# Kernel tuning notes

Measured on AMD Instinct MI355X. Metric: run time of the kernel, lower is better.

The kernel has to match this reference:

```python
import jax, jax.numpy as jnp
import numpy as np

B, H, W, C = 16, 64, 64, 256
WIN, SHIFT, HEADS, NSTYLE, HID = 8, 4, 8, 512, 1024
HB = HEADS // 2   # heads per attention branch
CB = C // 2       # channels per branch
N = WIN * WIN     # tokens per window
EPS = 1e-5


def _rel_index(w):
    coords = np.stack(np.meshgrid(np.arange(w), np.arange(w), indexing='ij'))  # [2,w,w]
    cf = coords.reshape(2, -1)
    rel = (cf[:, :, None] - cf[:, None, :]).transpose(1, 2, 0)  # [N,N,2]
    rel[:, :, 0] += w - 1
    rel[:, :, 1] += w - 1
    rel[:, :, 0] *= 2 * w - 1
    return rel.sum(-1)  # [N,N]


def _sw_mask(Hh, Ww, w, shift):
    img = np.zeros((Hh, Ww))
    cnt = 0
    for hs in (slice(0, -w), slice(-w, -shift), slice(-shift, None)):
        for ws in (slice(0, -w), slice(-w, -shift), slice(-shift, None)):
            img[hs, ws] = cnt
            cnt += 1
    win = img.reshape(Hh // w, w, Ww // w, w).transpose(0, 2, 1, 3).reshape(-1, w * w)
    m = win[:, None, :] - win[:, :, None]
    return np.where(m != 0, -100.0, 0.0).astype(np.float32)  # [nW,N,N]


REL_IDX = _rel_index(WIN)
SW_MASK = jnp.asarray(_sw_mask(H, W, WIN, SHIFT))


def window_partition(x):
    # x: [B,H,W,c] -> [B*nW, N, c]
    b, hh, ww, c = x.shape
    x = x.reshape(b, hh // WIN, WIN, ww // WIN, WIN, c).transpose(0, 1, 3, 2, 4, 5)
    return x.reshape(-1, N, c)


def window_reverse(win):
    c = win.shape[-1]
    x = win.reshape(B, H // WIN, W // WIN, WIN, WIN, c).transpose(0, 1, 3, 2, 4, 5)
    return x.reshape(B, H, W, c)


def _adain(x, style, Wa, ba):
    # x: [B,L,C]; instance norm over L per channel, then style affine
    s = style @ Wa + ba                      # [B, 2C]
    mu_s, std_s = jnp.split(s, 2, axis=1)    # each [B,C]
    mu = x.mean(axis=1, keepdims=True)
    var = ((x - mu) ** 2).mean(axis=1, keepdims=True)
    xn = (x - mu) * jax.lax.rsqrt(var + EPS)
    return mu_s[:, None, :] + std_s[:, None, :] * xn


def _win_attn(q, k, v, rpb, mask):
    # q,k,v: [B_, N, CB]; rpb: [(2w-1)^2, HB]; mask: [nW,N,N] or None
    B_ = q.shape[0]
    d = CB // HB
    q = q.reshape(B_, N, HB, d).transpose(0, 2, 1, 3) * (d ** -0.5)
    k = k.reshape(B_, N, HB, d).transpose(0, 2, 1, 3)
    v = v.reshape(B_, N, HB, d).transpose(0, 2, 1, 3)
    attn = jnp.einsum('bhnd,bhmd->bhnm', q, k)
    bias = rpb[REL_IDX.reshape(-1)].reshape(N, N, HB).transpose(2, 0, 1)
    attn = attn + bias[None]
    if mask is not None:
        nW = mask.shape[0]
        attn = attn.reshape(B_ // nW, nW, HB, N, N) + mask[None, :, None]
        attn = attn.reshape(B_, HB, N, N)
    attn = jax.nn.softmax(attn, axis=-1)
    out = jnp.einsum('bhnm,bhmd->bhnd', attn, v)
    return out.transpose(0, 2, 1, 3).reshape(B_, N, CB)


def setup_inputs() -> dict:
    key = jax.random.key(0)
    ks = jax.random.split(key, 20)
    f = jnp.float32
    return {
        'x': jax.random.normal(ks[0], (B, H * W, C), f),
        'style': jax.random.normal(ks[1], (B, NSTYLE), f),
        'w_qkv': jax.random.normal(ks[2], (C, 3 * C), f) * 0.02,
        'b_qkv': jnp.zeros((3 * C,), f),
        'w_proj': jax.random.normal(ks[3], (C, C), f) * 0.02,
        'b_proj': jnp.zeros((C,), f),
        'w_ada1': jax.random.normal(ks[4], (NSTYLE, 2 * C), f) * 0.02,
        'b_ada1': jnp.concatenate([jnp.zeros((C,), f), jnp.ones((C,), f)]),
        'w_ada2': jax.random.normal(ks[5], (NSTYLE, 2 * C), f) * 0.02,
        'b_ada2': jnp.concatenate([jnp.zeros((C,), f), jnp.ones((C,), f)]),
        'rpb1': jax.random.normal(ks[6], ((2 * WIN - 1) ** 2, HB), f) * 0.02,
        'rpb2': jax.random.normal(ks[7], ((2 * WIN - 1) ** 2, HB), f) * 0.02,
        'w_fc1': jax.random.normal(ks[8], (C, HID), f) * 0.02,
        'b_fc1': jnp.zeros((HID,), f),
        'w_fc2': jax.random.normal(ks[9], (HID, C), f) * 0.02,
        'b_fc2': jnp.zeros((C,), f),
    }


def reference(x, style, w_qkv, b_qkv, w_proj, b_proj, w_ada1, b_ada1,
              w_ada2, b_ada2, rpb1, rpb2, w_fc1, b_fc1, w_fc2, b_fc2):
    Bn, L, Cc = x.shape
    # AdaIN 1
    h = _adain(x, style, w_ada1, b_ada1)                      # [B,L,C]
    qkv = (h @ w_qkv + b_qkv).reshape(Bn, H, W, 3, Cc)
    q, k, v = qkv[..., 0, :], qkv[..., 1, :], qkv[..., 2, :]  # [B,H,W,C]
    # split channels across the two branches
    q1, k1, v1 = q[..., :CB], k[..., :CB], v[..., :CB]
    q2, k2, v2 = q[..., CB:], k[..., CB:], v[..., CB:]
    shift = lambda t: jnp.roll(t, (-SHIFT, -SHIFT), axis=(1, 2))
    # W-MSA branch
    x_w = _win_attn(window_partition(q1), window_partition(k1),
                    window_partition(v1), rpb1, None)
    # SW-MSA branch (shifted windows + mask)
    x_sw = _win_attn(window_partition(shift(q2)), window_partition(shift(k2)),
                     window_partition(shift(v2)), rpb2, SW_MASK)
    xw = window_reverse(x_w)                                  # [B,H,W,CB]
    xsw = jnp.roll(window_reverse(x_sw), (SHIFT, SHIFT), axis=(1, 2))
    attn_out = jnp.concatenate([xw, xsw], axis=-1).reshape(Bn, L, Cc)
    x = x + attn_out @ w_proj + b_proj
    # AdaIN 2 + MLP (exact GELU, as nn.GELU default)
    h2 = _adain(x, style, w_ada2, b_ada2)
    h2 = jax.nn.gelu(h2 @ w_fc1 + b_fc1, approximate=False)
    return x + (h2 @ w_fc2 + b_fc2)
```

## Files before the change

### kernel.cpp

```cpp
#include <hip/hip_runtime.h>
#include <hip/hip_bf16.h>

typedef __bf16 bf16;
typedef __bf16 bf16x4v __attribute__((ext_vector_type(4)));
typedef __bf16 bf16x8v __attribute__((ext_vector_type(8)));
typedef float f32x4 __attribute__((ext_vector_type(4)));
typedef short s16x4 __attribute__((ext_vector_type(4)));

#define DEVINL static __device__ __forceinline__
#define AS1 __attribute__((address_space(1)))
#define AS3 __attribute__((address_space(3)))

DEVINL f32x4 mfma16(bf16x8v a, bf16x8v b, f32x4 c) {
  return __builtin_amdgcn_mfma_f32_16x16x32_bf16(a, b, c, 0, 0, 0);
}

DEVINL f32x4 mfma16x16(bf16x4v a, bf16x4v b, f32x4 c) {
#if __has_builtin(__builtin_amdgcn_mfma_f32_16x16x16bf16_1k)
  return __builtin_amdgcn_mfma_f32_16x16x16bf16_1k(
      __builtin_bit_cast(s16x4, a), __builtin_bit_cast(s16x4, b), c, 0, 0, 0);
#else
  f32x4 d;
  asm("v_mfma_f32_16x16x16_bf16 %0, %1, %2, %3"
      : "=v"(d) : "v"(a), "v"(b), "v"(c));
  return d;
#endif
}

__global__ __launch_bounds__(256) void k_prep(
    const float* __restrict__ w_qkv, const float* __restrict__ w_proj,
    const float* __restrict__ w_fc1, const float* __restrict__ w_fc2,
    bf16* __restrict__ wtqkv, bf16* __restrict__ wtproj,
    bf16* __restrict__ wtfc1, bf16* __restrict__ wtfc2,
    const float* __restrict__ style,
    const float* __restrict__ wa1, const float* __restrict__ ba1,
    const float* __restrict__ wa2, const float* __restrict__ ba2,
    float* __restrict__ s1, float* __restrict__ s2,
    const float* __restrict__ x,
    float* __restrict__ psum, float* __restrict__ psq) {
  __shared__ float smem[32 * 33];
  int bid = blockIdx.x;
  int tid = threadIdx.x;

  if (bid < 768) {
    const float* in; bf16* out; int K, N, bx, by;
    if (bid < 192)      { in = w_qkv;  out = wtqkv;  K = 256;  N = 768;
                          bx = bid % 24;        by = bid / 24; }
    else if (bid < 256) { in = w_proj; out = wtproj; K = 256;  N = 256;
                          int i = bid - 192; bx = i % 8;  by = i / 8; }
    else if (bid < 512) { in = w_fc1;  out = wtfc1;  K = 256;  N = 1024;
                          int i = bid - 256; bx = i % 32; by = i / 32; }
    else                { in = w_fc2;  out = wtfc2;  K = 1024; N = 256;
                          int i = bid - 512; bx = i % 8;  by = i / 8; }
    float (*t)[33] = (float(*)[33])smem;
    int bx32 = bx * 32, by32 = by * 32;
    int tx = tid & 31, ty = tid >> 5;
    #pragma unroll
    for (int r = 0; r < 32; r += 8)
      t[ty + r][tx] = in[(size_t)(by32 + ty + r) * N + bx32 + tx];
    __syncthreads();
    #pragma unroll
    for (int r = 0; r < 32; r += 8)
      out[(size_t)(bx32 + ty + r) * K + by32 + tx] = (bf16)t[tx][ty + r];
  } else if (bid < 1792) {
    int i = bid - 768;
    int ng = i & 31, b = (i >> 5) & 15, which = i >> 9;
    int nl = tid & 15, kg = tid >> 4;
    int n = ng * 16 + nl;
    const float* wa = which ? wa2 : wa1;
    const float* ba = which ? ba2 : ba1;
    const float* srow = style + b * 512;
    float acc = 0.f;
    #pragma unroll 8
    for (int kk = 0; kk < 32; ++kk) {
      int k = kg + kk * 16;
      acc += srow[k] * wa[k * 512 + n];
    }
    acc += __shfl_xor(acc, 16);
    acc += __shfl_xor(acc, 32);
    float (*red)[16] = (float(*)[16])smem;
    int w = tid >> 6;
    if ((tid & 63) < 16) red[w][nl] = acc;
    __syncthreads();
    if (tid < 16) {
      float S = red[0][tid] + red[1][tid] + red[2][tid] + red[3][tid]
              + ba[ng * 16 + tid];
      (which ? s2 : s1)[b * 512 + ng * 16 + tid] = S;
    }
  } else {
    int i = bid - 1792;
    int rc = i & 63, b = i >> 6;
    int c = tid;
    size_t base = (size_t)b * 4096 * 256 + (size_t)rc * 64 * 256 + c;
    float sm = 0.f, q = 0.f;
    #pragma unroll 4
    for (int r = 0; r < 64; ++r) {
      float f = x[base + (size_t)r * 256];
      sm += f; q += f * f;
    }
    int o = (b * 64 + rc) * 256 + c;
    psum[o] = sm; psq[o] = q;
  }
}

__global__ __launch_bounds__(256) void k_stats_fin(
    const float* __restrict__ psum, const float* __restrict__ psq,
    const float* __restrict__ s,
    float* __restrict__ scale, float* __restrict__ shift) {
  int b = blockIdx.x, c = threadIdx.x;
  float S = 0.f, Q = 0.f;
  #pragma unroll 8
  for (int rc = 0; rc < 64; ++rc) {
    S += psum[(b * 64 + rc) * 256 + c];
    Q += psq[(b * 64 + rc) * 256 + c];
  }
  float mean = S * (1.0f/4096.0f);
  float var  = Q * (1.0f/4096.0f) - mean * mean;
  float inv  = rsqrtf(var + 1e-5f);
  float mu_s  = s[b * 512 + c];
  float std_s = s[b * 512 + 256 + c];
  float sc = std_s * inv;
  scale[b * 256 + c] = sc;
  shift[b * 256 + c] = mu_s - sc * mean;
}

__global__ __launch_bounds__(256) void k_stats_fin2(
    const float* __restrict__ pS, const float* __restrict__ pQ,
    const float* __restrict__ s,
    float* __restrict__ scale, float* __restrict__ shift) {
  int b = blockIdx.x, c = threadIdx.x;
  float S = 0.f, Q = 0.f;
  #pragma unroll 8
  for (int i = 0; i < 32; ++i) {
    S += pS[(b * 32 + i) * 256 + c];
    Q += pQ[(b * 32 + i) * 256 + c];
  }
  float mean = S * (1.0f/4096.0f);
  float var  = Q * (1.0f/4096.0f) - mean * mean;
  float inv  = rsqrtf(var + 1e-5f);
  float mu_s  = s[b * 512 + c];
  float std_s = s[b * 512 + 256 + c];
  float sc = std_s * inv;
  scale[b * 256 + c] = sc;
  shift[b * 256 + c] = mu_s - sc * mean;
}

template<int F32>
__global__ __launch_bounds__(256) void k_adain(
    const void* __restrict__ in, const float* __restrict__ scale,
    const float* __restrict__ shift, bf16* __restrict__ out) {
  int idx = blockIdx.x * 256 + threadIdx.x;
  int c8 = idx & 31, row = idx >> 5;
  int b = row >> 12, c = c8 * 8;
  const float* scp = &scale[b * 256 + c];
  const float* shp = &shift[b * 256 + c];
  f32x4 sc0 = *(const f32x4*)scp, sc1 = *(const f32x4*)(scp + 4);
  f32x4 sh0 = *(const f32x4*)shp, sh1 = *(const f32x4*)(shp + 4);
  size_t ofs = (size_t)row * 256 + c;
  float f[8];
  if constexpr (F32) {
    f32x4 v0 = *(const f32x4*)&((const float*)in)[ofs];
    f32x4 v1 = *(const f32x4*)&((const float*)in)[ofs + 4];
    f[0]=v0[0]; f[1]=v0[1]; f[2]=v0[2]; f[3]=v0[3];
    f[4]=v1[0]; f[5]=v1[1]; f[6]=v1[2]; f[7]=v1[3];
  } else {
    bf16x8v v = *(const bf16x8v*)&((const bf16*)in)[ofs];
    #pragma unroll
    for (int u = 0; u < 8; ++u) f[u] = (float)v[u];
  }
  bf16x8v o;
  o[0]=(bf16)(sh0[0]+sc0[0]*f[0]); o[1]=(bf16)(sh0[1]+sc0[1]*f[1]);
  o[2]=(bf16)(sh0[2]+sc0[2]*f[2]); o[3]=(bf16)(sh0[3]+sc0[3]*f[3]);
  o[4]=(bf16)(sh1[0]+sc1[0]*f[4]); o[5]=(bf16)(sh1[1]+sc1[1]*f[5]);
  o[6]=(bf16)(sh1[2]+sc1[2]*f[6]); o[7]=(bf16)(sh1[3]+sc1[3]*f[7]);
  *(bf16x8v*)&out[ofs] = o;
}

template<int RESMODE, int GELU, int OUTMODE>
__global__ __launch_bounds__(512) void k_gemm(
    const bf16* __restrict__ A, const bf16* __restrict__ Bt,
    const float* __restrict__ bias, const void* __restrict__ resv,
    void* __restrict__ outv, int N, int K, int gx) {
  __shared__ bf16 a_sw[256 * 64];
  __shared__ bf16 b_sw[128 * 64];
  int tid = threadIdx.x;
  int l = tid & 63, w = tid >> 6;
  int wr = w >> 1, wc = w & 1;
  int lm = l & 15, lg = l >> 4;

  int nwg = gridDim.x;
  int lin = blockIdx.x;
  int swz = (lin & 7) * (nwg >> 3) + (lin >> 3);
  int bx = swz % gx, by = swz / gx;
  int m0 = by * 256, n0 = bx * 128;

  f32x4 acc[4][4];
  #pragma unroll
  for (int mi = 0; mi < 4; ++mi)
    #pragma unroll
    for (int ni = 0; ni < 4; ++ni)
      acc[mi][ni] = (f32x4){0.f, 0.f, 0.f, 0.f};

  for (int k0 = 0; k0 < K; k0 += 64) {
    #pragma unroll
    for (int i = 0; i < 4; ++i) {
      int slot = i * 512 + tid;
      int r = slot >> 3, cs = slot & 7;
      int c = cs ^ (r & 7);
      const bf16* g = A + (size_t)(m0 + r) * K + k0 + c * 8;
      __builtin_amdgcn_global_load_lds(
          (const AS1 void*)g, (AS3 void*)(a_sw + (i * 512 + w * 64) * 8),
          16, 0, 0);
    }
    #pragma unroll
    for (int i = 0; i < 2; ++i) {
      int slot = i * 512 + tid;
      int r = slot >> 3, cs = slot & 7;
      int c = cs ^ (r & 7);
      const bf16* g = Bt + (size_t)(n0 + r) * K + k0 + c * 8;
      __builtin_amdgcn_global_load_lds(
          (const AS1 void*)g, (AS3 void*)(b_sw + (i * 512 + w * 64) * 8),
          16, 0, 0);
    }
    __syncthreads();
    #pragma unroll
    for (int kk = 0; kk < 2; ++kk) {
      bf16x8v af[4], bv[4];
      #pragma unroll
      for (int mi = 0; mi < 4; ++mi) {
        int row = wr * 64 + mi * 16 + lm;
        af[mi] = *(const bf16x8v*)&a_sw[row * 64 + (((kk * 4 + lg) ^ (row & 7)) * 8)];
      }
      #pragma unroll
      for (int ni = 0; ni < 4; ++ni) {
        int row = wc * 64 + ni * 16 + lm;
        bv[ni] = *(const bf16x8v*)&b_sw[row * 64 + (((kk * 4 + lg) ^ (row & 7)) * 8)];
      }
      #pragma unroll
      for (int mi = 0; mi < 4; ++mi)
        #pragma unroll
        for (int ni = 0; ni < 4; ++ni)
          acc[mi][ni] = mfma16(af[mi], bv[ni], acc[mi][ni]);
    }
    __syncthreads();
  }
  #pragma unroll
  for (int mi = 0; mi < 4; ++mi) {
    #pragma unroll
    for (int ni = 0; ni < 4; ++ni) {
      int row = m0 + wr * 64 + mi * 16 + lg * 4;
      int col = n0 + wc * 64 + ni * 16 + lm;
      float bv_ = bias[col];
      #pragma unroll
      for (int j = 0; j < 4; ++j) {
        float o = acc[mi][ni][j] + bv_;
        if constexpr (RESMODE == 1)
          o += ((const float*)resv)[(size_t)(row + j) * N + col];
        if constexpr (RESMODE == 2)
          o += (float)((const bf16*)resv)[(size_t)(row + j) * N + col];
        if constexpr (GELU) {
          float z = 1.5957691216057308f * (o + 0.044715f * o * o * o);
          o = o / (1.0f + __expf(-z));
        }
        if constexpr (OUTMODE == 1)
          ((float*)outv)[(size_t)(row + j) * N + col] = o;
        else if constexpr (OUTMODE == 2) {
          int b  = (row + j) >> 12, tok = (row + j) & 4095;
          int m  = col >> 8, c2 = col & 255;
          int hh = c2 >> 5, ch = c2 & 31;
          size_t a_ = ((size_t)((b * 3 + m) * 8 + hh) << 17) + (tok << 5) + ch;
          ((bf16*)outv)[a_] = (bf16)o;
        } else
          ((bf16*)outv)[(size_t)(row + j) * N + col] = (bf16)o;
      }
    }
  }
}

template<int RESMODE, int GELU, int OUTF32, int STATS>
__global__ __launch_bounds__(256) void k_gemm4(
    const bf16* __restrict__ A, const bf16* __restrict__ Bt,
    const float* __restrict__ bias, const void* __restrict__ resv,
    void* __restrict__ outv, int N, int K, int gx,
    float* __restrict__ pS, float* __restrict__ pQ) {
  __shared__ bf16 a_sw[128 * 64];
  __shared__ bf16 b_sw[128 * 64];
  int tid = threadIdx.x;
  int l = tid & 63, w = tid >> 6;
  int wr = w >> 1, wc = w & 1;
  int lm = l & 15, lg = l >> 4;

  int nwg = gridDim.x;
  int lin = blockIdx.x;
  int swz = (lin & 7) * (nwg >> 3) + (lin >> 3);
  int bx = swz % gx, by = swz / gx;
  int m0 = by * 128, n0 = bx * 128;

  f32x4 acc[4][4];
  #pragma unroll
  for (int mi = 0; mi < 4; ++mi)
    #pragma unroll
    for (int ni = 0; ni < 4; ++ni)
      acc[mi][ni] = (f32x4){0.f, 0.f, 0.f, 0.f};

  for (int k0 = 0; k0 < K; k0 += 64) {
    #pragma unroll
    for (int i = 0; i < 4; ++i) {
      int slot = i * 256 + tid;
      int r = slot >> 3, cs = slot & 7;
      int c = cs ^ (r & 7);
      __builtin_amdgcn_global_load_lds(
          (const AS1 void*)(A + (size_t)(m0 + r) * K + k0 + c * 8),
          (AS3 void*)(a_sw + (i * 256 + w * 64) * 8), 16, 0, 0);
    }
    #pragma unroll
    for (int i = 0; i < 4; ++i) {
      int slot = i * 256 + tid;
      int r = slot >> 3, cs = slot & 7;
      int c = cs ^ (r & 7);
      __builtin_amdgcn_global_load_lds(
          (const AS1 void*)(Bt + (size_t)(n0 + r) * K + k0 + c * 8),
          (AS3 void*)(b_sw + (i * 256 + w * 64) * 8), 16, 0, 0);
    }
    __syncthreads();
    #pragma unroll
    for (int kk = 0; kk < 2; ++kk) {
      bf16x8v af[4], bv[4];
      #pragma unroll
      for (int mi = 0; mi < 4; ++mi) {
        int row = wr * 64 + mi * 16 + lm;
        af[mi] = *(const bf16x8v*)&a_sw[row * 64 + (((kk * 4 + lg) ^ (row & 7)) * 8)];
      }
      #pragma unroll
      for (int ni = 0; ni < 4; ++ni) {
        int row = wc * 64 + ni * 16 + lm;
        bv[ni] = *(const bf16x8v*)&b_sw[row * 64 + (((kk * 4 + lg) ^ (row & 7)) * 8)];
      }
      #pragma unroll
      for (int mi = 0; mi < 4; ++mi)
        #pragma unroll
        for (int ni = 0; ni < 4; ++ni)
          acc[mi][ni] = mfma16(af[mi], bv[ni], acc[mi][ni]);
    }
    __syncthreads();
  }

  float sl[4] = {0.f, 0.f, 0.f, 0.f};
  float sq[4] = {0.f, 0.f, 0.f, 0.f};
  #pragma unroll
  for (int mi = 0; mi < 4; ++mi) {
    #pragma unroll
    for (int ni = 0; ni < 4; ++ni) {
      int row = m0 + wr * 64 + mi * 16 + lg * 4;
      int col = n0 + wc * 64 + ni * 16 + lm;
      float bv_ = bias[col];
      #pragma unroll
      for (int j = 0; j < 4; ++j) {
        float o = acc[mi][ni][j] + bv_;
        if constexpr (RESMODE == 1)
          o += ((const float*)resv)[(size_t)(row + j) * N + col];
        if constexpr (RESMODE == 2)
          o += (float)((const bf16*)resv)[(size_t)(row + j) * N + col];
        if constexpr (GELU) {
          float z = 1.5957691216057308f * (o + 0.044715f * o * o * o);
          o = o / (1.0f + __expf(-z));
        }
        if constexpr (OUTF32)
          ((float*)outv)[(size_t)(row + j) * N + col] = o;
        else
          ((bf16*)outv)[(size_t)(row + j) * N + col] = (bf16)o;
        if constexpr (STATS) {
          float ob = (float)(bf16)o;
          sl[ni] += ob;
          sq[ni] += ob * ob;
        }
      }
    }
  }

  if constexpr (STATS) {
    float* red = (float*)a_sw;
    #pragma unroll
    for (int ni = 0; ni < 4; ++ni) {
      int g = (wc * 4 + ni) * 16 + lm;
      red[g * 8 + wr * 4 + lg] = sl[ni];
      red[1024 + g * 8 + wr * 4 + lg] = sq[ni];
    }
    __syncthreads();
    if (tid < 128) {
      float S = 0.f, Q = 0.f;
      #pragma unroll
      for (int u = 0; u < 8; ++u) {
        S += red[tid * 8 + u];
        Q += red[1024 + tid * 8 + u];
      }
      pS[by * 256 + bx * 128 + tid] = S;
      pQ[by * 256 + bx * 128 + tid] = Q;
    }
  }
}

__global__ __launch_bounds__(256) void k_attn(
    const bf16* __restrict__ qkv,
    const float* __restrict__ rpb1, const float* __restrict__ rpb2,
    bf16* __restrict__ aout) {
  __shared__ bf16 vt[128 * 72];
  __shared__ float rl[960];

  int tid = threadIdx.x;
  int bx = blockIdx.x;
  int br = bx & 1, widx = (bx >> 1) & 63, b = bx >> 7;
  int wy = widx >> 3, wx = widx & 7;

  const float* rpb = br ? rpb2 : rpb1;
  #pragma unroll
  for (int t = tid; t < 960; t += 256) {
    int h0 = t / 240, r0 = t - h0 * 240, dy = r0 >> 4, dx = r0 & 15;
    rl[t] = (dx < 15) ? rpb[(dy * 15 + dx) * 4 + h0] : 0.f;
  }

  auto grow = [&](int tok) -> int {
    int y = wy * 8 + (tok >> 3), xc = wx * 8 + (tok & 7);
    if (br) { y = (y + 4) & 63; xc = (xc + 4) & 63; }
    return y * 64 + xc;
  };

  auto plane = [&](int m, int hh2) -> size_t {
    return (size_t)((b * 3 + m) * 8 + br * 4 + hh2) << 17;
  };

  #pragma unroll
  for (int it = 0; it < 4; ++it) {
    int task = it * 256 + tid;
    int tok = task >> 4, c = task & 15;
    int hh2 = c >> 2, ch8 = c & 3;
    bf16x8v v = *(const bf16x8v*)&qkv[plane(2, hh2) + (grow(tok) << 5) + ch8 * 8];
    int tsw = tok ^ ((c & 7) << 3);
    #pragma unroll
    for (int u = 0; u < 8; ++u) vt[(c * 8 + u) * 72 + tsw] = v[u];
  }

  int l = tid & 63, h = tid >> 6;
  int lm = l & 15, lg = l >> 4;

  bf16x8v kb[4], qa[4];
  size_t pq = plane(0, h), pk = plane(1, h);
  #pragma unroll
  for (int i = 0; i < 4; ++i) {
    int t = grow(i * 16 + lm);
    qa[i] = *(const bf16x8v*)&qkv[pq + (t << 5) + lg * 8];
    kb[i] = *(const bf16x8v*)&qkv[pk + (t << 5) + lg * 8];
  }
  __syncthreads();

  bf16x4v vb[2][4];
  #pragma unroll
  for (int ni = 0; ni < 2; ++ni)
    #pragma unroll
    for (int ki = 0; ki < 4; ++ki) {
      int row = h * 32 + ni * 16 + lm;
      int col = (ki * 16 + lg * 4) ^ (((row >> 3) & 7) << 3);
      vb[ni][ki] = *(const bf16x4v*)&vt[row * 72 + col];
    }

  bool need_mask = br && (wy == 7 || wx == 7);

  int ekA[16], idkA[16];
  #pragma unroll
  for (int ki = 0; ki < 4; ++ki)
    #pragma unroll
    for (int j = 0; j < 4; ++j) {
      int ik = ki * 16 + lg * 4 + j;
      ekA[ki * 4 + j] = ik + (ik >> 3) * 8;
      int yk = wy * 8 + (ik >> 3), xk = wx * 8 + (ik & 7);
      idkA[ki * 4 + j] = (yk < 56 ? 0 : (yk < 60 ? 1 : 2)) * 3
                       + (xk < 56 ? 0 : (xk < 60 ? 1 : 2));
    }

  #pragma unroll
  for (int qi = 0; qi < 4; ++qi) {
    f32x4 s[4];
    #pragma unroll
    for (int ki = 0; ki < 4; ++ki)
      s[ki] = mfma16(kb[ki], qa[qi], (f32x4){0.f,0.f,0.f,0.f});

    int iq = qi * 16 + lm;
    int eq = iq + (iq >> 3) * 8;
    int yq = wy * 8 + (iq >> 3), xq = wx * 8 + (iq & 7);
    int idq = (yq < 56 ? 0 : (yq < 60 ? 1 : 2)) * 3
            + (xq < 56 ? 0 : (xq < 60 ? 1 : 2));
    const float* fb = &rl[h * 240 + 119 + eq];

    #pragma unroll
    for (int ki = 0; ki < 4; ++ki)
      #pragma unroll
      for (int j = 0; j < 4; ++j) {
        float val = s[ki][j] * 0.17677669529663687f + fb[-ekA[ki * 4 + j]];
        if (need_mask && idq != idkA[ki * 4 + j]) val -= 100.0f;
        s[ki][j] = val;
      }

    float mx = s[0][0];
    #pragma unroll
    for (int ki = 0; ki < 4; ++ki)
      #pragma unroll
      for (int j = 0; j < 4; ++j) mx = fmaxf(mx, s[ki][j]);
    mx = fmaxf(mx, __shfl_xor(mx, 16));
    mx = fmaxf(mx, __shfl_xor(mx, 32));
    float sum = 0.f;
    #pragma unroll
    for (int ki = 0; ki < 4; ++ki)
      #pragma unroll
      for (int j = 0; j < 4; ++j) {
        float e = __expf(s[ki][j] - mx);
        s[ki][j] = e;
        sum += e;
      }
    sum += __shfl_xor(sum, 16);
    sum += __shfl_xor(sum, 32);
    float rs = 1.0f / sum;

    bf16x4v pa[4];
    #pragma unroll
    for (int ki = 0; ki < 4; ++ki)
      #pragma unroll
      for (int j = 0; j < 4; ++j)
        pa[ki][j] = (bf16)(s[ki][j] * rs);

    f32x4 o[2] = {(f32x4){0.f,0.f,0.f,0.f}, (f32x4){0.f,0.f,0.f,0.f}};
    #pragma unroll
    for (int ki = 0; ki < 4; ++ki) {
      o[0] = mfma16x16(pa[ki], vb[0][ki], o[0]);
      o[1] = mfma16x16(pa[ki], vb[1][ki], o[1]);
    }

    #pragma unroll
    for (int ni = 0; ni < 2; ++ni)
      #pragma unroll
      for (int j = 0; j < 4; ++j) {
        int tok = qi * 16 + lg * 4 + j;
        int col = br * 128 + h * 32 + ni * 16 + lm;
        aout[((size_t)b * 4096 + grow(tok)) * 256 + col] = (bf16)o[ni][j];
      }
  }
}

extern "C" void kernel_launch(void* const* d_in, const int* in_sizes, int n_in,
                              void* d_out, int out_size, void* d_ws, size_t ws_size,
                              hipStream_t stream) {
  (void)in_sizes; (void)n_in; (void)out_size; (void)ws_size;
  const float* x      = (const float*)d_in[0];
  const float* style  = (const float*)d_in[1];
  const float* w_qkv  = (const float*)d_in[2];
  const float* b_qkv  = (const float*)d_in[3];
  const float* w_proj = (const float*)d_in[4];
  const float* b_proj = (const float*)d_in[5];
  const float* w_ada1 = (const float*)d_in[6];
  const float* b_ada1 = (const float*)d_in[7];
  const float* w_ada2 = (const float*)d_in[8];
  const float* b_ada2 = (const float*)d_in[9];
  const float* rpb1   = (const float*)d_in[10];
  const float* rpb2   = (const float*)d_in[11];
  const float* w_fc1  = (const float*)d_in[12];
  const float* b_fc1  = (const float*)d_in[13];
  const float* w_fc2  = (const float*)d_in[14];
  const float* b_fc2  = (const float*)d_in[15];

  char* ws = (char*)d_ws;
  float* s1     = (float*)(ws + 0);
  float* s2     = (float*)(ws + 32768);
  float* scale1 = (float*)(ws + 65536);
  float* shift1 = (float*)(ws + 81920);
  float* scale2 = (float*)(ws + 98304);
  float* shift2 = (float*)(ws + 114688);
  bf16* wtqkv   = (bf16*)(ws + 131072);
  bf16* wtproj  = (bf16*)(ws + 524288);
  bf16* wtfc1   = (bf16*)(ws + 655360);
  bf16* wtfc2   = (bf16*)(ws + 1179648);
  float* psum   = (float*)(ws + 1703936);
  float* psq    = (float*)(ws + 2752512);
  float* pS     = (float*)(ws + 1703936);
  const size_t BIG = 4194304;
  bf16* xn   = (bf16*)(ws + BIG);
  bf16* qkv  = (bf16*)(ws + BIG + 33554432);
  bf16* attn = (bf16*)(ws + BIG + 134217728);
  bf16* x1   = (bf16*)(ws + BIG + 33554432);
  bf16* xn2  = xn;
  bf16* g    = (bf16*)(ws + BIG + 67108864);
  float* pQ  = (float*)(ws + BIG + 167772160);

  k_prep<<<2816, 256, 0, stream>>>(
      w_qkv, w_proj, w_fc1, w_fc2, wtqkv, wtproj, wtfc1, wtfc2,
      style, w_ada1, b_ada1, w_ada2, b_ada2, s1, s2, x, psum, psq);

  k_stats_fin<<<16, 256, 0, stream>>>(psum, psq, s1, scale1, shift1);
  k_adain<1><<<8192, 256, 0, stream>>>(x, scale1, shift1, xn);

  k_gemm<0,0,2><<<1536, 512, 0, stream>>>(
      xn, wtqkv, b_qkv, nullptr, qkv, 768, 256, 6);

  k_attn<<<2048, 256, 0, stream>>>(qkv, rpb1, rpb2, attn);

  k_gemm4<1,0,0,1><<<1024, 256, 0, stream>>>(
      attn, wtproj, b_proj, x, x1, 256, 256, 2, pS, pQ);

  k_stats_fin2<<<16, 256, 0, stream>>>(pS, pQ, s2, scale2, shift2);
  k_adain<0><<<8192, 256, 0, stream>>>(x1, scale2, shift2, xn2);

  for (int ch = 0; ch < 2; ++ch) {
    size_t ro = (size_t)ch * 32768;
    k_gemm<0,1,0><<<1024, 512, 0, stream>>>(
        xn2 + ro * 256, wtfc1, b_fc1, nullptr, g, 1024, 256, 8);
    k_gemm4<2,0,1,0><<<512, 256, 0, stream>>>(
        g, wtfc2, b_fc2, x1 + ro * 256,
        (float*)d_out + ro * 256, 256, 1024, 2, nullptr, nullptr);
  }
}
```

Baseline: 285.4 us.

## Fold second AdaIN affine into per-batch scaled fc1 weights and bias

Rather than materialising a normalized copy of x1 before fc1, a new kernel builds per-batch fc1 weights scaled by the AdaIN scale, plus a per-batch bias that absorbs the shift term. The fc1 GEMM then reads x1 directly and picks the batch's weight slice from its row block. This removes a full elementwise pass over the activation tensor (one read and one write). In exchange it adds a small weight-scaling kernel, 16 copies of the fc1 weights with less L2 reuse, and bf16 rounding applied to the scaled weights rather than to the normalized activations.

```diff
diff --git a/kernel.cpp b/kernel.cpp
--- a/kernel.cpp
+++ b/kernel.cpp
@@ -145,9 +145,42 @@
   shift[b * 256 + c] = mu_s - sc * mean;
 }
 
-template<int F32>
+__global__ __launch_bounds__(256) void k_scalew(
+    const bf16* __restrict__ wt, const float* __restrict__ bias,
+    const float* __restrict__ scale, const float* __restrict__ shift,
+    bf16* __restrict__ wout, float* __restrict__ bout, int N) {
+  int b = blockIdx.y;
+  int n = blockIdx.x * 16 + (threadIdx.x >> 4);
+  int kg = threadIdx.x & 15;
+  const bf16* wrow = wt + (size_t)n * 256 + kg * 16;
+  const float* sc = scale + b * 256 + kg * 16;
+  const float* sh = shift + b * 256 + kg * 16;
+  bf16* orow = wout + ((size_t)b * N + n) * 256 + kg * 16;
+  float dot = 0.f;
+  bf16x8v w0 = *(const bf16x8v*)wrow;
+  bf16x8v w1 = *(const bf16x8v*)(wrow + 8);
+  bf16x8v o0, o1;
+  #pragma unroll
+  for (int u = 0; u < 8; ++u) {
+    float wv = (float)w0[u];
+    o0[u] = (bf16)(sc[u] * wv);
+    dot += sh[u] * wv;
+  }
+  #pragma unroll
+  for (int u = 0; u < 8; ++u) {
+    float wv = (float)w1[u];
+    o1[u] = (bf16)(sc[8 + u] * wv);
+    dot += sh[8 + u] * wv;
+  }
+  *(bf16x8v*)orow = o0;
+  *(bf16x8v*)(orow + 8) = o1;
+  #pragma unroll
+  for (int m = 1; m <= 8; m <<= 1) dot += __shfl_xor(dot, m);
+  if (kg == 0) bout[b * N + n] = bias[n] + dot;
+}
+
 __global__ __launch_bounds__(256) void k_adain(
-    const void* __restrict__ in, const float* __restrict__ scale,
+    const float* __restrict__ in, const float* __restrict__ scale,
     const float* __restrict__ shift, bf16* __restrict__ out) {
   int idx = blockIdx.x * 256 + threadIdx.x;
   int c8 = idx & 31, row = idx >> 5;
@@ -157,30 +190,21 @@
   f32x4 sc0 = *(const f32x4*)scp, sc1 = *(const f32x4*)(scp + 4);
   f32x4 sh0 = *(const f32x4*)shp, sh1 = *(const f32x4*)(shp + 4);
   size_t ofs = (size_t)row * 256 + c;
-  float f[8];
-  if constexpr (F32) {
-    f32x4 v0 = *(const f32x4*)&((const float*)in)[ofs];
-    f32x4 v1 = *(const f32x4*)&((const float*)in)[ofs + 4];
-    f[0]=v0[0]; f[1]=v0[1]; f[2]=v0[2]; f[3]=v0[3];
-    f[4]=v1[0]; f[5]=v1[1]; f[6]=v1[2]; f[7]=v1[3];
-  } else {
-    bf16x8v v = *(const bf16x8v*)&((const bf16*)in)[ofs];
-    #pragma unroll
-    for (int u = 0; u < 8; ++u) f[u] = (float)v[u];
-  }
+  f32x4 v0 = *(const f32x4*)&in[ofs];
+  f32x4 v1 = *(const f32x4*)&in[ofs + 4];
   bf16x8v o;
-  o[0]=(bf16)(sh0[0]+sc0[0]*f[0]); o[1]=(bf16)(sh0[1]+sc0[1]*f[1]);
-  o[2]=(bf16)(sh0[2]+sc0[2]*f[2]); o[3]=(bf16)(sh0[3]+sc0[3]*f[3]);
-  o[4]=(bf16)(sh1[0]+sc1[0]*f[4]); o[5]=(bf16)(sh1[1]+sc1[1]*f[5]);
-  o[6]=(bf16)(sh1[2]+sc1[2]*f[6]); o[7]=(bf16)(sh1[3]+sc1[3]*f[7]);
+  o[0]=(bf16)(sh0[0]+sc0[0]*v0[0]); o[1]=(bf16)(sh0[1]+sc0[1]*v0[1]);
+  o[2]=(bf16)(sh0[2]+sc0[2]*v0[2]); o[3]=(bf16)(sh0[3]+sc0[3]*v0[3]);
+  o[4]=(bf16)(sh1[0]+sc1[0]*v1[0]); o[5]=(bf16)(sh1[1]+sc1[1]*v1[1]);
+  o[6]=(bf16)(sh1[2]+sc1[2]*v1[2]); o[7]=(bf16)(sh1[3]+sc1[3]*v1[3]);
   *(bf16x8v*)&out[ofs] = o;
 }
 
-template<int RESMODE, int GELU, int OUTMODE>
+template<int GELU, int OUTMODE, int BPERB>
 __global__ __launch_bounds__(512) void k_gemm(
     const bf16* __restrict__ A, const bf16* __restrict__ Bt,
-    const float* __restrict__ bias, const void* __restrict__ resv,
-    void* __restrict__ outv, int N, int K, int gx) {
+    const float* __restrict__ bias,
+    void* __restrict__ outv, int N, int K, int gx, int row_off) {
   __shared__ bf16 a_sw[256 * 64];
   __shared__ bf16 b_sw[128 * 64];
   int tid = threadIdx.x;
@@ -193,6 +217,11 @@
   int swz = (lin & 7) * (nwg >> 3) + (lin >> 3);
   int bx = swz % gx, by = swz / gx;
   int m0 = by * 256, n0 = bx * 128;
+
+  int bb = 0;
+  if constexpr (BPERB) bb = (m0 + row_off) >> 12;
+  const bf16* BtX = Bt + (size_t)bb * ((size_t)N * K);
+  const float* biasX = bias + bb * N;
 
   f32x4 acc[4][4];
   #pragma unroll
@@ -217,7 +246,7 @@
       int slot = i * 512 + tid;
       int r = slot >> 3, cs = slot & 7;
       int c = cs ^ (r & 7);
-      const bf16* g = Bt + (size_t)(n0 + r) * K + k0 + c * 8;
+      const bf16* g = BtX + (size_t)(n0 + r) * K + k0 + c * 8;
       __builtin_amdgcn_global_load_lds(
           (const AS1 void*)g, (AS3 void*)(b_sw + (i * 512 + w * 64) * 8),
           16, 0, 0);
@@ -250,21 +279,15 @@
     for (int ni = 0; ni < 4; ++ni) {
       int row = m0 + wr * 64 + mi * 16 + lg * 4;
       int col = n0 + wc * 64 + ni * 16 + lm;
-      float bv_ = bias[col];
+      float bv_ = biasX[col];
       #pragma unroll
       for (int j = 0; j < 4; ++j) {
         float o = acc[mi][ni][j] + bv_;
-        if constexpr (RESMODE == 1)
-          o += ((const float*)resv)[(size_t)(row + j) * N + col];
-        if constexpr (RESMODE == 2)
-          o += (float)((const bf16*)resv)[(size_t)(row + j) * N + col];
         if constexpr (GELU) {
           float z = 1.5957691216057308f * (o + 0.044715f * o * o * o);
           o = o / (1.0f + __expf(-z));
         }
-        if constexpr (OUTMODE == 1)
-          ((float*)outv)[(size_t)(row + j) * N + col] = o;
-        else if constexpr (OUTMODE == 2) {
+        if constexpr (OUTMODE == 2) {
           int b  = (row + j) >> 12, tok = (row + j) & 4095;
           int m  = col >> 8, c2 = col & 255;
           int hh = c2 >> 5, ch = c2 & 31;
@@ -580,12 +603,13 @@
   float* psum   = (float*)(ws + 1703936);
   float* psq    = (float*)(ws + 2752512);
   float* pS     = (float*)(ws + 1703936);
+  float* bfc1s  = (float*)(ws + 2752512);
   const size_t BIG = 4194304;
-  bf16* xn   = (bf16*)(ws + BIG);
+  bf16* xn    = (bf16*)(ws + BIG);
+  bf16* wfc1s = (bf16*)(ws + BIG);
   bf16* qkv  = (bf16*)(ws + BIG + 33554432);
   bf16* attn = (bf16*)(ws + BIG + 134217728);
   bf16* x1   = (bf16*)(ws + BIG + 33554432);
-  bf16* xn2  = xn;
   bf16* g    = (bf16*)(ws + BIG + 67108864);
   float* pQ  = (float*)(ws + BIG + 167772160);
 
@@ -594,10 +618,10 @@
       style, w_ada1, b_ada1, w_ada2, b_ada2, s1, s2, x, psum, psq);
 
   k_stats_fin<<<16, 256, 0, stream>>>(psum, psq, s1, scale1, shift1);
-  k_adain<1><<<8192, 256, 0, stream>>>(x, scale1, shift1, xn);
-
-  k_gemm<0,0,2><<<1536, 512, 0, stream>>>(
-      xn, wtqkv, b_qkv, nullptr, qkv, 768, 256, 6);
+  k_adain<<<8192, 256, 0, stream>>>(x, scale1, shift1, xn);
+
+  k_gemm<0,2,0><<<1536, 512, 0, stream>>>(
+      xn, wtqkv, b_qkv, qkv, 768, 256, 6, 0);
 
   k_attn<<<2048, 256, 0, stream>>>(qkv, rpb1, rpb2, attn);
 
@@ -605,12 +629,13 @@
       attn, wtproj, b_proj, x, x1, 256, 256, 2, pS, pQ);
 
   k_stats_fin2<<<16, 256, 0, stream>>>(pS, pQ, s2, scale2, shift2);
-  k_adain<0><<<8192, 256, 0, stream>>>(x1, scale2, shift2, xn2);
+  k_scalew<<<dim3(64, 16), 256, 0, stream>>>(
+      wtfc1, b_fc1, scale2, shift2, wfc1s, bfc1s, 1024);
 
   for (int ch = 0; ch < 2; ++ch) {
     size_t ro = (size_t)ch * 32768;
-    k_gemm<0,1,0><<<1024, 512, 0, stream>>>(
-        xn2 + ro * 256, wtfc1, b_fc1, nullptr, g, 1024, 256, 8);
+    k_gemm<1,0,1><<<1024, 512, 0, stream>>>(
+        x1 + ro * 256, wfc1s, bfc1s, g, 1024, 256, 8, (int)ro);
     k_gemm4<2,0,1,0><<<512, 256, 0, stream>>>(
         g, wtfc2, b_fc2, x1 + ro * 256,
         (float*)d_out + ro * 256, 256, 1024, 2, nullptr, nullptr);
```

Measured after the change: 280.3 us. Within noise of the previous version (-1.8%).
